# Kernel optimization log

Hardware: AMD Instinct MI355X
Metric: run time of the kernel (lower is better)

The kernel has to match this reference:

```python
import jax, jax.numpy as jnp
import numpy as np


def setup_inputs() -> dict:
    key = jax.random.key(0)
    k1, k2 = jax.random.split(key)
    B, N, M = 8, 8192, 8192
    xyz1 = jax.random.normal(k1, (B, N, 3), dtype=jnp.float32)
    xyz2 = jax.random.normal(k2, (B, M, 3), dtype=jnp.float32)
    return {"xyz1": xyz1, "xyz2": xyz2}


def reference(xyz1, xyz2):
    # (same math as the CUDA kernel's per-pair squared L2 scan).
    sq1 = jnp.sum(xyz1 * xyz1, axis=-1)              # [B, N]
    sq2 = jnp.sum(xyz2 * xyz2, axis=-1)              # [B, M]
    inner = jnp.einsum('bnd,bmd->bnm', xyz1, xyz2)   # [B, N, M]
    d = sq1[:, :, None] + sq2[:, None, :] - 2.0 * inner
    d = jnp.maximum(d, 0.0)  # guard tiny negatives from the expansion
    dist1 = jnp.min(d, axis=2)  # [B, N] nearest sq-dist in xyz2 for each xyz1 point
    dist2 = jnp.min(d, axis=1)  # [B, M] nearest sq-dist in xyz1 for each xyz2 point
    return dist1, dist2
```

## Files before the change

kernel.cpp:

```cpp
#include <hip/hip_runtime.h>
#include <math.h>


typedef __attribute__((ext_vector_type(8))) short short8;
typedef __attribute__((ext_vector_type(16))) float f32x16;

#define NSPLIT 4
#define QPW    64
#define QPB    (QPW * 4)

__host__ __device__ static inline size_t pad512(size_t x) {
  return (x + 511) & ~(size_t)511;
}

__device__ __forceinline__ unsigned short bf16h(float x) {
  unsigned u = __float_as_uint(x);
  return (unsigned short)((u + 0x7fffu + ((u >> 16) & 1u)) >> 16);
}
__device__ __forceinline__ float bf16f(unsigned short h) {
  return __uint_as_float((unsigned)h << 16);
}
__device__ __forceinline__ float m3(float a, float b, float c) {
  return fminf(fminf(a, b), c);
}
__device__ __forceinline__ float red16(const f32x16& d, float mm) {
  float r0 = m3(d[0], d[1], d[2]);
  float r1 = m3(d[3], d[4], d[5]);
  float r2 = m3(d[6], d[7], d[8]);
  float r3 = m3(d[9], d[10], d[11]);
  float r4 = m3(d[12], d[13], d[14]);
  return m3(m3(r0, r1, r2), m3(r3, r4, d[15]), mm);
}

__global__ __launch_bounds__(256) void frag_kernel(
    const float* __restrict__ xyz1, const float* __restrict__ xyz2,
    char* __restrict__ frags, float* __restrict__ out, int B, int N, int M)
{
  const int z = blockIdx.z, dir = z / B, b = z % B;
  const size_t Mpad = pad512((size_t)M), Npad = pad512((size_t)N);
  const float* cp; char* reg_; int Nc; size_t Pc; float* oreg; int NqO;
  if (dir == 0) {
    cp = xyz2 + (size_t)b * M * 3;
    reg_ = frags + (size_t)b * Mpad * 32;
    Nc = M; Pc = Mpad;
    oreg = out + (size_t)b * N; NqO = N;
  } else {
    cp = xyz1 + (size_t)b * N * 3;
    reg_ = frags + (size_t)B * Mpad * 32 + (size_t)b * Npad * 32;
    Nc = N; Pc = Npad;
    oreg = out + (size_t)B * N + (size_t)b * M; NqO = M;
  }
  const size_t j = (size_t)blockIdx.x * 256 + threadIdx.x;

  if (j < (size_t)NqO) ((unsigned*)oreg)[j] = 0x7f7f7f7fu;
  if (j >= Pc) return;

  float x = 0.f, y = 0.f, zz = 0.f, sq = 3.0e38f;
  if (j < (size_t)Nc) {
    x = cp[3 * j + 0]; y = cp[3 * j + 1]; zz = cp[3 * j + 2];
    sq = x * x; sq = fmaf(y, y, sq); sq = fmaf(zz, zz, sq);
  }
  const float ex = -2.f * x, ey = -2.f * y, ez = -2.f * zz;
  const unsigned short ehx = bf16h(ex); const unsigned short elx = bf16h(ex - bf16f(ehx));
  const unsigned short ehy = bf16h(ey); const unsigned short ely = bf16h(ey - bf16f(ehy));
  const unsigned short ehz = bf16h(ez); const unsigned short elz = bf16h(ez - bf16f(ehz));
  const unsigned short sh  = bf16h(sq); const unsigned short sl  = bf16h(sq - bf16f(sh));

  short8 f0, f1;
  f0[0] = (short)ehx; f0[1] = (short)ehy; f0[2] = (short)ehz; f0[3] = (short)elx;
  f0[4] = (short)ely; f0[5] = (short)elz; f0[6] = (short)ehx; f0[7] = (short)ehy;
  f1[0] = (short)ehz; f1[1] = (short)elx; f1[2] = (short)ely; f1[3] = (short)elz;
  f1[4] = (short)sh;  f1[5] = (short)sl;  f1[6] = 0;          f1[7] = 0;

  short8* fp = (short8*)reg_ + ((j >> 5) * 64 + (j & 31));
  fp[0]  = f0;
  fp[32] = f1;
}

__device__ __forceinline__ short8 make_qfrag(float x, float y, float z, int hi) {
  const unsigned short hx = bf16h(x); const unsigned short lx = bf16h(x - bf16f(hx));
  const unsigned short hy = bf16h(y); const unsigned short ly = bf16h(y - bf16f(hy));
  const unsigned short hz = bf16h(z); const unsigned short lz = bf16h(z - bf16f(hz));
  const unsigned short ONE = 0x3F80;
  short8 f;
  if (hi == 0) {
    f[0] = (short)hx; f[1] = (short)hy; f[2] = (short)hz; f[3] = (short)hx;
    f[4] = (short)hy; f[5] = (short)hz; f[6] = (short)lx; f[7] = (short)ly;
  } else {
    f[0] = (short)lz; f[1] = (short)lx; f[2] = (short)ly; f[3] = (short)lz;
    f[4] = (short)ONE; f[5] = (short)ONE; f[6] = 0; f[7] = 0;
  }
  return f;
}

#define GROUP_BODY(fcur, gofs)                                                \
  {                                                                           \
    f32x16 d0 = __builtin_amdgcn_mfma_f32_32x32x16_bf16(fcur, bq0, zacc, 0, 0, 0); \
    f32x16 d1 = __builtin_amdgcn_mfma_f32_32x32x16_bf16(fcur, bq1, zacc, 0, 0, 0); \
    mm0 = red16(d0, mm0);                                                     \
    mm1 = red16(d1, mm1);                                                     \
    fcur = *(const short8*)(gp + (size_t)(gofs) * 1024);                      \
  }

__global__ __launch_bounds__(256, 6) void chamfer_mfma(
    const float* __restrict__ xyz1, const float* __restrict__ xyz2,
    const char* __restrict__ frags, float* __restrict__ out,
    int B, int N, int M)
{
  const int id   = (int)blockIdx.x;
  const int z    = id % (2 * B);
  const int rest = id / (2 * B);
  const int by   = rest % NSPLIT;
  const int bx   = rest / NSPLIT;

  const int dir = z / B, b = z % B;
  const size_t Mpad = pad512((size_t)M), Npad = pad512((size_t)N);
  const float* qp; float* o; const char* fr; int Nq, Nc;
  if (dir == 0) {
    qp = xyz1 + (size_t)b * N * 3;
    o  = out + (size_t)b * N;
    fr = frags + (size_t)b * Mpad * 32;
    Nq = N; Nc = (int)Mpad;
  } else {
    qp = xyz2 + (size_t)b * M * 3;
    o  = out + (size_t)B * N + (size_t)b * M;
    fr = frags + (size_t)B * Mpad * 32 + (size_t)b * Npad * 32;
    Nq = M; Nc = (int)Npad;
  }
  if (bx * QPB >= Nq) return;

  const int lane = threadIdx.x & 63;
  const int wid  = threadIdx.x >> 6;
  const int hi   = lane >> 5;

  const int gq = Nc / (32 * NSPLIT);
  const char* gp = fr + (size_t)by * gq * 1024 + (size_t)lane * 16;

  const int qbase = bx * QPB + wid * QPW;
  const int n0 = qbase + (lane & 31);
  const int n1 = n0 + 32;
  const int n0c = n0 < Nq ? n0 : Nq - 1;
  const int n1c = n1 < Nq ? n1 : Nq - 1;
  const float q0x = qp[3 * n0c], q0y = qp[3 * n0c + 1], q0z = qp[3 * n0c + 2];
  const float q1x = qp[3 * n1c], q1y = qp[3 * n1c + 1], q1z = qp[3 * n1c + 2];
  float sqq0 = q0x * q0x; sqq0 = fmaf(q0y, q0y, sqq0); sqq0 = fmaf(q0z, q0z, sqq0);
  float sqq1 = q1x * q1x; sqq1 = fmaf(q1y, q1y, sqq1); sqq1 = fmaf(q1z, q1z, sqq1);
  const short8 bq0 = make_qfrag(q0x, q0y, q0z, hi);
  const short8 bq1 = make_qfrag(q1x, q1y, q1z, hi);

  const f32x16 zacc = {0.f,0.f,0.f,0.f,0.f,0.f,0.f,0.f,
                       0.f,0.f,0.f,0.f,0.f,0.f,0.f,0.f};
  float mm0 = 3.0e38f, mm1 = 3.0e38f;

  short8 f0 = *(const short8*)(gp);
  short8 f1 = *(const short8*)(gp + 1024);
#pragma unroll 1
  for (int g = 0; g < gq; g += 2) {
    GROUP_BODY(f0, g + 2)
    GROUP_BODY(f1, g + 3)
  }

  mm0 = fminf(mm0, __shfl_xor(mm0, 32));
  mm1 = fminf(mm1, __shfl_xor(mm1, 32));
  if (lane < 32) {
    if (n0 < Nq) atomicMin((unsigned int*)(o + n0), __float_as_uint(fmaxf(mm0 + sqq0, 0.f)));
    if (n1 < Nq) atomicMin((unsigned int*)(o + n1), __float_as_uint(fmaxf(mm1 + sqq1, 0.f)));
  }
}

extern "C" void kernel_launch(void* const* d_in, const int* in_sizes, int n_in,
                              void* d_out, int out_size, void* d_ws, size_t ws_size,
                              hipStream_t stream) {
  const float* xyz1 = (const float*)d_in[0];
  const float* xyz2 = (const float*)d_in[1];
  float* out = (float*)d_out;

  const int B = 8;
  const int N = in_sizes[0] / (B * 3);
  const int M = in_sizes[1] / (B * 3);

  const size_t Npad = pad512((size_t)N), Mpad = pad512((size_t)M);
  char* frags = (char*)d_ws;

  const size_t pmax = Npad > Mpad ? Npad : Mpad;
  dim3 g1((unsigned)(pmax / 256), 1, 2 * B);
  frag_kernel<<<g1, dim3(256), 0, stream>>>(xyz1, xyz2, frags, out, B, N, M);

  const int nmax = N > M ? N : M;
  const unsigned nx = (unsigned)((nmax + QPB - 1) / QPB);
  dim3 g2(nx * NSPLIT * 2 * B, 1, 1);
  chamfer_mfma<<<g2, dim3(256), 0, stream>>>(xyz1, xyz2, frags, out, B, N, M);
}
```

Measured before the change: 89.56 us.

## Process eight query fragments per wave to reuse candidate fragments across MFMAs

Raises queries per wave from 64 to 256, so each loaded candidate fragment feeds eight MFMAs and eight running minima instead of two. This cuts global/L2 fragment traffic and loop overhead per MFMA. In exchange, register pressure rises, launch bounds drop to 2 blocks per CU, and the grid shrinks fourfold. That may reduce occupancy and latency hiding.

New measurement: 90.94 us. About the same (+1.5%).

```diff
diff --git a/kernel.cpp b/kernel.cpp
--- a/kernel.cpp
+++ b/kernel.cpp
@@ -6,7 +6,7 @@
 typedef __attribute__((ext_vector_type(16))) float f32x16;
 
 #define NSPLIT 4
-#define QPW    64
+#define QPW    256
 #define QPB    (QPW * 4)
 
 __host__ __device__ static inline size_t pad512(size_t x) {
@@ -97,12 +97,24 @@
   {                                                                           \
     f32x16 d0 = __builtin_amdgcn_mfma_f32_32x32x16_bf16(fcur, bq0, zacc, 0, 0, 0); \
     f32x16 d1 = __builtin_amdgcn_mfma_f32_32x32x16_bf16(fcur, bq1, zacc, 0, 0, 0); \
+    f32x16 d2 = __builtin_amdgcn_mfma_f32_32x32x16_bf16(fcur, bq2, zacc, 0, 0, 0); \
+    f32x16 d3 = __builtin_amdgcn_mfma_f32_32x32x16_bf16(fcur, bq3, zacc, 0, 0, 0); \
+    f32x16 d4 = __builtin_amdgcn_mfma_f32_32x32x16_bf16(fcur, bq4, zacc, 0, 0, 0); \
+    f32x16 d5 = __builtin_amdgcn_mfma_f32_32x32x16_bf16(fcur, bq5, zacc, 0, 0, 0); \
+    f32x16 d6 = __builtin_amdgcn_mfma_f32_32x32x16_bf16(fcur, bq6, zacc, 0, 0, 0); \
+    f32x16 d7 = __builtin_amdgcn_mfma_f32_32x32x16_bf16(fcur, bq7, zacc, 0, 0, 0); \
+    fcur = *(const short8*)(gp + (size_t)(gofs) * 1024);                      \
     mm0 = red16(d0, mm0);                                                     \
     mm1 = red16(d1, mm1);                                                     \
-    fcur = *(const short8*)(gp + (size_t)(gofs) * 1024);                      \
-  }
-
-__global__ __launch_bounds__(256, 6) void chamfer_mfma(
+    mm2 = red16(d2, mm2);                                                     \
+    mm3 = red16(d3, mm3);                                                     \
+    mm4 = red16(d4, mm4);                                                     \
+    mm5 = red16(d5, mm5);                                                     \
+    mm6 = red16(d6, mm6);                                                     \
+    mm7 = red16(d7, mm7);                                                     \
+  }
+
+__global__ __launch_bounds__(256, 2) void chamfer_mfma(
     const float* __restrict__ xyz1, const float* __restrict__ xyz2,
     const char* __restrict__ frags, float* __restrict__ out,
     int B, int N, int M)
@@ -137,20 +149,24 @@
   const char* gp = fr + (size_t)by * gq * 1024 + (size_t)lane * 16;
 
   const int qbase = bx * QPB + wid * QPW;
-  const int n0 = qbase + (lane & 31);
-  const int n1 = n0 + 32;
-  const int n0c = n0 < Nq ? n0 : Nq - 1;
-  const int n1c = n1 < Nq ? n1 : Nq - 1;
-  const float q0x = qp[3 * n0c], q0y = qp[3 * n0c + 1], q0z = qp[3 * n0c + 2];
-  const float q1x = qp[3 * n1c], q1y = qp[3 * n1c + 1], q1z = qp[3 * n1c + 2];
-  float sqq0 = q0x * q0x; sqq0 = fmaf(q0y, q0y, sqq0); sqq0 = fmaf(q0z, q0z, sqq0);
-  float sqq1 = q1x * q1x; sqq1 = fmaf(q1y, q1y, sqq1); sqq1 = fmaf(q1z, q1z, sqq1);
-  const short8 bq0 = make_qfrag(q0x, q0y, q0z, hi);
-  const short8 bq1 = make_qfrag(q1x, q1y, q1z, hi);
+  int nn[8]; float sqq[8]; short8 bq[8];
+#pragma unroll
+  for (int k = 0; k < 8; ++k) {
+    const int n = qbase + (lane & 31) + 32 * k;
+    nn[k] = n;
+    const int nc = n < Nq ? n : Nq - 1;
+    const float qx = qp[3 * nc], qy = qp[3 * nc + 1], qz = qp[3 * nc + 2];
+    float s = qx * qx; s = fmaf(qy, qy, s); s = fmaf(qz, qz, s);
+    sqq[k] = s;
+    bq[k] = make_qfrag(qx, qy, qz, hi);
+  }
+  const short8 bq0 = bq[0], bq1 = bq[1], bq2 = bq[2], bq3 = bq[3];
+  const short8 bq4 = bq[4], bq5 = bq[5], bq6 = bq[6], bq7 = bq[7];
 
   const f32x16 zacc = {0.f,0.f,0.f,0.f,0.f,0.f,0.f,0.f,
                        0.f,0.f,0.f,0.f,0.f,0.f,0.f,0.f};
-  float mm0 = 3.0e38f, mm1 = 3.0e38f;
+  float mm0 = 3.0e38f, mm1 = 3.0e38f, mm2 = 3.0e38f, mm3 = 3.0e38f;
+  float mm4 = 3.0e38f, mm5 = 3.0e38f, mm6 = 3.0e38f, mm7 = 3.0e38f;
 
   short8 f0 = *(const short8*)(gp);
   short8 f1 = *(const short8*)(gp + 1024);
@@ -160,11 +176,12 @@
     GROUP_BODY(f1, g + 3)
   }
 
-  mm0 = fminf(mm0, __shfl_xor(mm0, 32));
-  mm1 = fminf(mm1, __shfl_xor(mm1, 32));
-  if (lane < 32) {
-    if (n0 < Nq) atomicMin((unsigned int*)(o + n0), __float_as_uint(fmaxf(mm0 + sqq0, 0.f)));
-    if (n1 < Nq) atomicMin((unsigned int*)(o + n1), __float_as_uint(fmaxf(mm1 + sqq1, 0.f)));
+  float mm[8] = {mm0, mm1, mm2, mm3, mm4, mm5, mm6, mm7};
+#pragma unroll
+  for (int k = 0; k < 8; ++k) {
+    float v = fminf(mm[k], __shfl_xor(mm[k], 32));
+    if (lane < 32 && nn[k] < Nq)
+      atomicMin((unsigned int*)(o + nn[k]), __float_as_uint(fmaxf(v + sqq[k], 0.f)));
   }
 }
 
```
